# Kernel optimization log

Measured on AMD Instinct MI355X. Metric: run time of the kernel, lower is better.

The kernel has to match this reference:

```python
import jax, jax.numpy as jnp
import numpy as np

N_NODES = 100000
N_EDGES = 1600000
N_GRAPHS = 1024
IN_CH = 64
HID = 32
H4, H2 = HID * 4, HID * 2


def _glorot(key, shape):
    fan_in, fan_out = shape[0], shape[1]
    lim = (6.0 / (fan_in + fan_out)) ** 0.5
    return jax.random.uniform(key, shape, jnp.float32, -lim, lim)


def setup_inputs() -> dict:
    key = jax.random.key(0)
    ks = jax.random.split(key, 32)
    inp = {
        "x": jax.random.normal(ks[0], (N_NODES, IN_CH), jnp.float32),
        "edge_index": jax.random.randint(ks[1], (2, N_EDGES), 0, N_NODES, jnp.int64),
        "batch": jnp.sort(jax.random.randint(ks[2], (N_NODES,), 0, N_GRAPHS, jnp.int64)),
    }
    dims = [(IN_CH, H4), (H4, H2), (H2, H2), (H2, H2)]
    for i, (di, do) in enumerate(dims, 1):
        inp[f"c{i}_wl"] = _glorot(ks[3 * i], (di, do))
        inp[f"c{i}_bl"] = jnp.zeros((do,), jnp.float32)
        inp[f"c{i}_wr"] = _glorot(ks[3 * i + 1], (di, do))
    lin_dims = [(H2, H2), (H2, HID), (HID, HID), (HID, 1)]
    for i, (di, do) in enumerate(lin_dims, 1):
        inp[f"lin{i}_w"] = _glorot(ks[15 + 2 * i], (di, do))
        inp[f"lin{i}_b"] = jnp.zeros((do,), jnp.float32)
    return inp


def _sage(x, src, dst, wl, bl, wr):
    # mean-aggregate neighbor (source) features at target nodes
    agg = jax.ops.segment_sum(x[src], dst, num_segments=N_NODES)
    deg = jax.ops.segment_sum(jnp.ones((src.shape[0],), x.dtype), dst, num_segments=N_NODES)
    agg = agg / jnp.maximum(deg, 1.0)[:, None]
    return agg @ wl + bl + x @ wr


def reference(x, edge_index, batch,
              c1_wl, c1_bl, c1_wr, c2_wl, c2_bl, c2_wr,
              c3_wl, c3_bl, c3_wr, c4_wl, c4_bl, c4_wr,
              lin1_w, lin1_b, lin2_w, lin2_b, lin3_w, lin3_b, lin4_w, lin4_b):
    src, dst = edge_index[0], edge_index[1]
    h = jax.nn.relu(_sage(x, src, dst, c1_wl, c1_bl, c1_wr))
    h = jax.nn.relu(_sage(h, src, dst, c2_wl, c2_bl, c2_wr))
    h = jax.nn.relu(_sage(h, src, dst, c3_wl, c3_bl, c3_wr))
    h = jax.nn.relu(_sage(h, src, dst, c4_wl, c4_bl, c4_wr))
    # global mean pool over graphs
    gsum = jax.ops.segment_sum(h, batch, num_segments=N_GRAPHS)
    gcnt = jax.ops.segment_sum(jnp.ones((h.shape[0],), h.dtype), batch, num_segments=N_GRAPHS)
    g = gsum / jnp.maximum(gcnt, 1.0)[:, None]
    g = jax.nn.relu(g @ lin1_w + lin1_b)
    g = jax.nn.relu(g @ lin2_w + lin2_b)
    g = jax.nn.relu(g @ lin3_w + lin3_b)
    out = (g @ lin4_w + lin4_b).squeeze(1)  # [N_GRAPHS]
    return out
```

## Files before the change

### kernel.cpp

```cpp
#include <hip/hip_runtime.h>

#define NN 100000
#define NE 1600000
#define NG 1024
#define CPAD 4
#define MAXDEG 64

#define GB_COUNT 6250
#define GB_Z     1563
#define GB_CVT   3125
#define GB_BND   5
#define GB_PREP  320
#define GB_SETUP (2 * GB_COUNT)

typedef __attribute__((ext_vector_type(8))) short bf16x8;
typedef __attribute__((ext_vector_type(4))) float f32x4;

__device__ __forceinline__ unsigned f2bf1(float f) {
  union { float f; unsigned u; } v; v.f = f;
  return (v.u + 0x7fffu + ((v.u >> 16) & 1u)) >> 16;
}
__device__ __forceinline__ unsigned packbf2(float a, float b) {
  return f2bf1(a) | (f2bf1(b) << 16);
}
__device__ __forceinline__ float bflo(unsigned u) {
  union { unsigned u; float f; } v; v.u = u << 16; return v.f;
}
__device__ __forceinline__ float bfhi(unsigned u) {
  union { unsigned u; float f; } v; v.u = u & 0xffff0000u; return v.f;
}
__device__ __forceinline__ float bfs(unsigned short s) {
  union { unsigned u; float f; } v; v.u = ((unsigned)s) << 16; return v.f;
}

#define ACC16(A, P0, P1)                                              \
  A[0] += bflo(P0.x); A[1] += bfhi(P0.x);                             \
  A[2] += bflo(P0.y); A[3] += bfhi(P0.y);                             \
  A[4] += bflo(P0.z); A[5] += bfhi(P0.z);                             \
  A[6] += bflo(P0.w); A[7] += bfhi(P0.w);                             \
  A[8] += bflo(P1.x); A[9] += bfhi(P1.x);                             \
  A[10] += bflo(P1.y); A[11] += bfhi(P1.y);                           \
  A[12] += bflo(P1.z); A[13] += bfhi(P1.z);                           \
  A[14] += bflo(P1.w); A[15] += bfhi(P1.w);

#define ACC8(A, V)                                                    \
  A[0] += bflo(V.x); A[1] += bfhi(V.x);                               \
  A[2] += bflo(V.y); A[3] += bfhi(V.y);                               \
  A[4] += bflo(V.z); A[5] += bfhi(V.z);                               \
  A[6] += bflo(V.w); A[7] += bfhi(V.w);

__global__ __launch_bounds__(256) void k_prepz(const float* __restrict__ c1wr,
                                               unsigned short* __restrict__ pLZ) {
  int e = blockIdx.x * 256 + threadIdx.x;
  if (e >= 64 * 128) return;
  int k = e >> 7, n = e & 127;
  int t = k >> 5, kq = (k >> 3) & 3, j = k & 7;
  int n0 = n >> 4, nl = n & 15;
  pLZ[((((n0 * 2 + t) * 64) + (kq * 16 + nl)) << 3) + j] =
      (unsigned short)f2bf1(c1wr[k * 128 + n]);
}

__global__ __launch_bounds__(256) void k_setup(
    const int* __restrict__ src, const int* __restrict__ dst,
    int* __restrict__ cnt, int* __restrict__ csr,
    const float* __restrict__ X, unsigned short* __restrict__ Xb,
    const int* __restrict__ batch, int* __restrict__ gstart,
    const unsigned short* __restrict__ pLZ, const float* __restrict__ c1bl,
    unsigned short* __restrict__ ZZ,
    const float* __restrict__ c1wl, const float* __restrict__ c1wr,
    const float* __restrict__ c2wl, const float* __restrict__ c2wr,
    const float* __restrict__ c3wl, const float* __restrict__ c3wr,
    const float* __restrict__ c4wl, const float* __restrict__ c4wr,
    unsigned short* __restrict__ pL1, unsigned short* __restrict__ pL2a,
    unsigned short* __restrict__ pL2b, unsigned short* __restrict__ pL3,
    unsigned short* __restrict__ pL4) {
  __shared__ __align__(16) char smem[64 * 66 * 4];
  int b = blockIdx.x, tid = threadIdx.x;

  if ((b & 1) == 0) {
    int e = (b >> 1) * 256 + tid;
    int d = dst[e];
    int s = src[e];
    int r = atomicAdd(&cnt[(size_t)d * CPAD], 1);
    if (r < MAXDEG) csr[d * MAXDEG + r] = s;
    return;
  }
  int ob = b >> 1;

  if (ob < GB_Z) {
    unsigned short* sA = (unsigned short*)smem;
    float* sC = (float*)smem;
    const int m0 = ob * 64;
#pragma unroll
    for (int l = 0; l < 2; ++l) {
      int c = tid + l * 256;
      int m = c >> 3, k8 = c & 7;
      int row = m0 + m;
      uint4 o = make_uint4(0, 0, 0, 0);
      if (row < NN) {
        const float4* xp = (const float4*)(X + (size_t)row * 64 + k8 * 8);
        float4 p0 = xp[0], p1 = xp[1];
        o.x = packbf2(p0.x, p0.y); o.y = packbf2(p0.z, p0.w);
        o.z = packbf2(p1.x, p1.y); o.w = packbf2(p1.z, p1.w);
      }
      int wv = m >> 4, mr = m & 15, t = k8 >> 2, kq = k8 & 3;
      ((uint4*)sA)[(wv * 2 + t) * 64 + kq * 16 + mr] = o;
    }
    __syncthreads();
    const int w = tid >> 6, L = tid & 63;
    const bf16x8* Af = (const bf16x8*)sA;
    const bf16x8* Bf = (const bf16x8*)pLZ;
    f32x4 acc[8];
#pragma unroll
    for (int i = 0; i < 8; ++i)
#pragma unroll
      for (int j = 0; j < 4; ++j) acc[i][j] = 0.f;
#pragma unroll
    for (int t = 0; t < 2; ++t) {
      bf16x8 afr = Af[(w * 2 + t) * 64 + L];
#pragma unroll
      for (int n0 = 0; n0 < 8; ++n0) {
        bf16x8 bfr = Bf[(n0 * 2 + t) * 64 + L];
        acc[n0] = __builtin_amdgcn_mfma_f32_16x16x32_bf16(afr, bfr, acc[n0], 0, 0, 0);
      }
    }
    int rg = L >> 4, cl = L & 15;
#pragma unroll
    for (int half = 0; half < 2; ++half) {
      __syncthreads();
#pragma unroll
      for (int n0 = 0; n0 < 4; ++n0)
#pragma unroll
        for (int r = 0; r < 4; ++r)
          sC[(w * 16 + rg * 4 + r) * 66 + n0 * 16 + cl] = acc[half * 4 + n0][r];
      __syncthreads();
#pragma unroll
      for (int it = 0; it < 2; ++it) {
        int c = tid + it * 256;
        int m = c >> 3, c8 = c & 7;
        int row = m0 + m;
        if (row < NN) {
          float v[8];
#pragma unroll
          for (int j = 0; j < 8; ++j)
            v[j] = sC[m * 66 + c8 * 8 + j] + c1bl[half * 64 + c8 * 8 + j];
          uint4 o;
          o.x = packbf2(v[0], v[1]); o.y = packbf2(v[2], v[3]);
          o.z = packbf2(v[4], v[5]); o.w = packbf2(v[6], v[7]);
          ((uint4*)(ZZ + (size_t)row * 128 + half * 64))[c8] = o;
        }
      }
    }
    return;
  }
  ob -= GB_Z;
  if (ob < GB_CVT) {
    int i = ob * 256 + tid;
    const float4* p = (const float4*)X + (size_t)i * 2;
    float4 a = p[0], c = p[1];
    uint4 o;
    o.x = packbf2(a.x, a.y); o.y = packbf2(a.z, a.w);
    o.z = packbf2(c.x, c.y); o.w = packbf2(c.z, c.w);
    ((uint4*)Xb)[i] = o;
    return;
  }
  ob -= GB_CVT;
  if (ob < GB_BND) {
    int g = ob * 256 + tid;
    if (g > NG) return;
    int lo = 0, hi = NN;
    while (lo < hi) {
      int mid = (lo + hi) >> 1;
      if (batch[mid] < g) lo = mid + 1; else hi = mid;
    }
    gstart[g] = lo;
    return;
  }
  ob -= GB_BND;
  if (ob < GB_PREP) {
    int yb = ob >> 6, xb = ob & 63;
    const float *WL, *WR; unsigned short* dstp; int N;
    if (yb == 0)      { WL = c1wl; WR = c1wr;           dstp = pL1;  N = 128; }
    else if (yb == 1) { WL = c2wl; WR = c2wl + 64 * 64; dstp = pL2a; N = 64; }
    else if (yb == 2) { WL = c2wr; WR = c2wr + 64 * 64; dstp = pL2b; N = 64; }
    else if (yb == 3) { WL = c3wl; WR = c3wr;           dstp = pL3;  N = 64; }
    else              { WL = c4wl; WR = c4wr;           dstp = pL4;  N = 64; }
    int e = xb * 256 + tid;
    if (e >= 128 * N) return;
    int k = e / N, n = e - k * N;
    float w = (k < 64) ? WL[k * N + n] : WR[(k - 64) * N + n];
    int t = k >> 5, kq = (k >> 3) & 3, j = k & 7;
    int n0 = n >> 4, nl = n & 15;
    dstp[((((n0 * 4 + t) * 64) + (kq * 16 + nl)) << 3) + j] =
        (unsigned short)f2bf1(w);
  }
}

__global__ __launch_bounds__(256) void k_gather(
    const unsigned short* __restrict__ F, const int* __restrict__ csr,
    const int* __restrict__ cnt, const float* __restrict__ bias,
    const unsigned short* __restrict__ Z, unsigned short* __restrict__ out) {
  int idx = blockIdx.x * 256 + threadIdx.x;
  int n = idx >> 3, q = idx & 7;
  int deg = cnt[(size_t)n * CPAD];
  int degc = min(deg, MAXDEG);
  int beg = n * MAXDEG, end = beg + degc;
  float aA[8], aB[8];
#pragma unroll
  for (int c = 0; c < 8; ++c) { aA[c] = 0.f; aB[c] = 0.f; }
  int e = beg;
  for (; e + 8 <= end; e += 8) {
    int4 s0 = *(const int4*)(csr + e);
    int4 s1 = *(const int4*)(csr + e + 4);
    uint4 v0 = ((const uint4*)(F + (size_t)s0.x * 64))[q];
    uint4 v1 = ((const uint4*)(F + (size_t)s0.y * 64))[q];
    uint4 v2 = ((const uint4*)(F + (size_t)s0.z * 64))[q];
    uint4 v3 = ((const uint4*)(F + (size_t)s0.w * 64))[q];
    uint4 v4 = ((const uint4*)(F + (size_t)s1.x * 64))[q];
    uint4 v5 = ((const uint4*)(F + (size_t)s1.y * 64))[q];
    uint4 v6 = ((const uint4*)(F + (size_t)s1.z * 64))[q];
    uint4 v7 = ((const uint4*)(F + (size_t)s1.w * 64))[q];
    ACC8(aA, v0) ACC8(aB, v1) ACC8(aA, v2) ACC8(aB, v3)
    ACC8(aA, v4) ACC8(aB, v5) ACC8(aA, v6) ACC8(aB, v7)
  }
  if (e + 4 <= end) {
    int4 s0 = *(const int4*)(csr + e);
    uint4 v0 = ((const uint4*)(F + (size_t)s0.x * 64))[q];
    uint4 v1 = ((const uint4*)(F + (size_t)s0.y * 64))[q];
    uint4 v2 = ((const uint4*)(F + (size_t)s0.z * 64))[q];
    uint4 v3 = ((const uint4*)(F + (size_t)s0.w * 64))[q];
    ACC8(aA, v0) ACC8(aB, v1) ACC8(aA, v2) ACC8(aB, v3)
    e += 4;
  }
  for (; e < end; ++e) {
    uint4 v0 = ((const uint4*)(F + (size_t)csr[e] * 64))[q];
    ACC8(aA, v0)
  }
  float a[8];
  float iv = 1.0f / fmaxf((float)deg, 1.0f);
#pragma unroll
  for (int c = 0; c < 8; ++c) a[c] = (aA[c] + aB[c]) * iv;
  {
    uint4 z = ((const uint4*)(Z + (size_t)n * 64))[q];
    const float4* bp = (const float4*)(bias + q * 8);
    float4 b0 = bp[0], b1 = bp[1];
    a[0] = fmaxf(a[0] + b0.x + bflo(z.x), 0.f);
    a[1] = fmaxf(a[1] + b0.y + bfhi(z.x), 0.f);
    a[2] = fmaxf(a[2] + b0.z + bflo(z.y), 0.f);
    a[3] = fmaxf(a[3] + b0.w + bfhi(z.y), 0.f);
    a[4] = fmaxf(a[4] + b1.x + bflo(z.z), 0.f);
    a[5] = fmaxf(a[5] + b1.y + bfhi(z.z), 0.f);
    a[6] = fmaxf(a[6] + b1.z + bflo(z.w), 0.f);
    a[7] = fmaxf(a[7] + b1.w + bfhi(z.w), 0.f);
  }
  uint4 o;
  o.x = packbf2(a[0], a[1]); o.y = packbf2(a[2], a[3]);
  o.z = packbf2(a[4], a[5]); o.w = packbf2(a[6], a[7]);
  ((uint4*)(out + (size_t)n * 64))[q] = o;
}

__device__ __forceinline__ void gather_row(
    const unsigned short* __restrict__ F, const int* __restrict__ csr,
    const int* __restrict__ cnt, int row, int qr, float* a0) {
  float a1[16];
#pragma unroll
  for (int c = 0; c < 16; ++c) { a0[c] = 0.f; a1[c] = 0.f; }
  int deg = cnt[(size_t)row * CPAD];
  int degc = min(deg, MAXDEG);
  int beg = row * MAXDEG, end = beg + degc;
  int e = beg;
  for (; e + 4 <= end; e += 4) {
    int4 ss = *(const int4*)(csr + e);
    const uint4* r0 = (const uint4*)(F + (size_t)ss.x * 64) + qr * 2;
    const uint4* r1 = (const uint4*)(F + (size_t)ss.y * 64) + qr * 2;
    const uint4* r2 = (const uint4*)(F + (size_t)ss.z * 64) + qr * 2;
    const uint4* r3 = (const uint4*)(F + (size_t)ss.w * 64) + qr * 2;
    uint4 p0 = r0[0], p1 = r0[1], q0 = r1[0], q1 = r1[1];
    uint4 p2 = r2[0], p3 = r2[1], q2 = r3[0], q3 = r3[1];
    ACC16(a0, p0, p1) ACC16(a1, q0, q1)
    ACC16(a0, p2, p3) ACC16(a1, q2, q3)
  }
  if (e + 2 <= end) {
    int s0 = csr[e], s1 = csr[e + 1];
    const uint4* r0 = (const uint4*)(F + (size_t)s0 * 64) + qr * 2;
    const uint4* r1 = (const uint4*)(F + (size_t)s1 * 64) + qr * 2;
    uint4 p0 = r0[0], p1 = r0[1], q0 = r1[0], q1 = r1[1];
    ACC16(a0, p0, p1) ACC16(a1, q0, q1)
    e += 2;
  }
  if (e < end) {
    const uint4* r0 = (const uint4*)(F + (size_t)csr[e] * 64) + qr * 2;
    uint4 p0 = r0[0], p1 = r0[1];
    ACC16(a0, p0, p1)
  }
  float iv = 1.0f / fmaxf((float)deg, 1.0f);
#pragma unroll
  for (int c = 0; c < 16; ++c) a0[c] = (a0[c] + a1[c]) * iv;
}

__global__ __launch_bounds__(256, 4) void k_fgemm1(
    const unsigned short* __restrict__ F, const int* __restrict__ csr,
    const int* __restrict__ cnt,
    const unsigned short* __restrict__ Wp,
    const unsigned short* __restrict__ ZZ,
    const unsigned short* __restrict__ Wa,
    const unsigned short* __restrict__ Wb,
    unsigned short* __restrict__ OUTa,
    unsigned short* __restrict__ OUTb) {
  __shared__ __align__(16) char smem[64 * 66 * 4 + 64 * 128 * 2];
  unsigned short* sA = (unsigned short*)smem;
  float* sC = (float*)smem;
  unsigned short* sA2 = (unsigned short*)(smem + 64 * 66 * 4);
  const int tid = threadIdx.x;
  const int m0 = blockIdx.x * 64;

  {
    int m = tid >> 2, qr = tid & 3;
    int row = m0 + m;
    float a0[16];
    if (row < NN) {
      gather_row(F, csr, cnt, row, qr, a0);
    } else {
#pragma unroll
      for (int c = 0; c < 16; ++c) a0[c] = 0.f;
    }
    int wv = m >> 4, mr = m & 15;
#pragma unroll
    for (int h = 0; h < 2; ++h) {
      int k8 = qr * 2 + h;
      int t = k8 >> 2, kq = k8 & 3;
      uint4 o;
      o.x = packbf2(a0[h * 8 + 0], a0[h * 8 + 1]);
      o.y = packbf2(a0[h * 8 + 2], a0[h * 8 + 3]);
      o.z = packbf2(a0[h * 8 + 4], a0[h * 8 + 5]);
      o.w = packbf2(a0[h * 8 + 6], a0[h * 8 + 7]);
      ((uint4*)sA)[(wv * 2 + t) * 64 + kq * 16 + mr] = o;
    }
  }
  __syncthreads();

  const int w = tid >> 6, L = tid & 63;
  const bf16x8* Af = (const bf16x8*)sA;
  const bf16x8* Bf = (const bf16x8*)Wp;
  f32x4 acc[8];
#pragma unroll
  for (int i = 0; i < 8; ++i)
#pragma unroll
    for (int j = 0; j < 4; ++j) acc[i][j] = 0.f;
#pragma unroll
  for (int t = 0; t < 2; ++t) {
    bf16x8 afr = Af[(w * 2 + t) * 64 + L];
#pragma unroll
    for (int n0 = 0; n0 < 8; ++n0) {
      bf16x8 bfr = Bf[(n0 * 4 + t) * 64 + L];
      acc[n0] = __builtin_amdgcn_mfma_f32_16x16x32_bf16(afr, bfr, acc[n0], 0, 0, 0);
    }
  }

  int rg = L >> 4, cl = L & 15;
#pragma unroll
  for (int half = 0; half < 2; ++half) {
    __syncthreads();
#pragma unroll
    for (int n0 = 0; n0 < 4; ++n0)
#pragma unroll
      for (int r = 0; r < 4; ++r)
        sC[(w * 16 + rg * 4 + r) * 66 + n0 * 16 + cl] = acc[half * 4 + n0][r];
    __syncthreads();
#pragma unroll
    for (int it = 0; it < 2; ++it) {
      int c = tid + it * 256;
      int m = c >> 3, c8 = c & 7;
      int row = m0 + m;
      uint4 o = make_uint4(0, 0, 0, 0);
      if (row < NN) {
        uint4 z = ((const uint4*)(ZZ + (size_t)row * 128 + half * 64))[c8];
        float zb[8] = {bflo(z.x), bfhi(z.x), bflo(z.y), bfhi(z.y),
                       bflo(z.z), bfhi(z.z), bflo(z.w), bfhi(z.w)};
        float v[8];
#pragma unroll
        for (int j = 0; j < 8; ++j)
          v[j] = fmaxf(sC[m * 66 + c8 * 8 + j] + zb[j], 0.f);
        o.x = packbf2(v[0], v[1]); o.y = packbf2(v[2], v[3]);
        o.z = packbf2(v[4], v[5]); o.w = packbf2(v[6], v[7]);
      }
      int k8 = half * 8 + c8, t = k8 >> 2, kq = k8 & 3;
      int wv = m >> 4, mr = m & 15;
      ((uint4*)sA2)[(wv * 4 + t) * 64 + kq * 16 + mr] = o;
    }
  }
  __syncthreads();

  const bf16x8* A2 = (const bf16x8*)sA2;
  const bf16x8* Ba = (const bf16x8*)Wa;
  const bf16x8* Bb = (const bf16x8*)Wb;
  f32x4 ca[4], cb[4];
#pragma unroll
  for (int i = 0; i < 4; ++i)
#pragma unroll
    for (int j = 0; j < 4; ++j) { ca[i][j] = 0.f; cb[i][j] = 0.f; }
#pragma unroll
  for (int t = 0; t < 4; ++t) {
    bf16x8 afr = A2[(w * 4 + t) * 64 + L];
#pragma unroll
    for (int n0 = 0; n0 < 4; ++n0) {
      ca[n0] = __builtin_amdgcn_mfma_f32_16x16x32_bf16(afr, Ba[(n0 * 4 + t) * 64 + L], ca[n0], 0, 0, 0);
      cb[n0] = __builtin_amdgcn_mfma_f32_16x16x32_bf16(afr, Bb[(n0 * 4 + t) * 64 + L], cb[n0], 0, 0, 0);
    }
  }
#pragma unroll
  for (int s = 0; s < 2; ++s) {
    unsigned short* OUT = s ? OUTb : OUTa;
    __syncthreads();
#pragma unroll
    for (int n0 = 0; n0 < 4; ++n0)
#pragma unroll
      for (int r = 0; r < 4; ++r)
        sC[(w * 16 + rg * 4 + r) * 66 + n0 * 16 + cl] =
            s ? cb[n0][r] : ca[n0][r];
    __syncthreads();
#pragma unroll
    for (int it = 0; it < 2; ++it) {
      int c = tid + it * 256;
      int m = c >> 3, c8 = c & 7;
      int row = m0 + m;
      if (row < NN) {
        float v[8];
#pragma unroll
        for (int j = 0; j < 8; ++j) v[j] = sC[m * 66 + c8 * 8 + j];
        uint4 o;
        o.x = packbf2(v[0], v[1]); o.y = packbf2(v[2], v[3]);
        o.z = packbf2(v[4], v[5]); o.w = packbf2(v[6], v[7]);
        ((uint4*)(OUT + (size_t)row * 64))[c8] = o;
      }
    }
  }
}

template <int NF>
__global__ __launch_bounds__(256, 4) void k_fgemm(
    const unsigned short* __restrict__ F, const int* __restrict__ csr,
    const int* __restrict__ cnt,
    const unsigned short* __restrict__ Wp, const float* __restrict__ bias,
    unsigned short* __restrict__ OUT, int outStride) {
  __shared__ __align__(16) char smem[64 * 66 * 4];
  unsigned short* sA = (unsigned short*)smem;
  float* sC = (float*)smem;
  const int tid = threadIdx.x;
  const int m0 = blockIdx.x * 64;

  {
    int m = tid >> 2, qr = tid & 3;
    int row = m0 + m;
    float a0[16];
    if (row < NN) {
      gather_row(F, csr, cnt, row, qr, a0);
    } else {
#pragma unroll
      for (int c = 0; c < 16; ++c) a0[c] = 0.f;
    }
    int wv = m >> 4, mr = m & 15;
#pragma unroll
    for (int h = 0; h < 2; ++h) {
      int k8 = qr * 2 + h;
      int t = k8 >> 2, kq = k8 & 3;
      uint4 o;
      o.x = packbf2(a0[h * 8 + 0], a0[h * 8 + 1]);
      o.y = packbf2(a0[h * 8 + 2], a0[h * 8 + 3]);
      o.z = packbf2(a0[h * 8 + 4], a0[h * 8 + 5]);
      o.w = packbf2(a0[h * 8 + 6], a0[h * 8 + 7]);
      ((uint4*)sA)[(wv * 4 + t) * 64 + kq * 16 + mr] = o;
    }
  }
#pragma unroll
  for (int l = 0; l < 2; ++l) {
    int c = tid + l * 256;
    int m = c >> 3, j = c & 7;
    int row = m0 + m;
    uint4 v = make_uint4(0, 0, 0, 0);
    if (row < NN) v = ((const uint4*)(F + (size_t)row * 64))[j];
    int k8 = 8 + j, t = k8 >> 2, kq = k8 & 3;
    int wv = m >> 4, mr = m & 15;
    ((uint4*)sA)[(wv * 4 + t) * 64 + kq * 16 + mr] = v;
  }
  __syncthreads();

  const int w = tid >> 6, L = tid & 63;
  const bf16x8* Af = (const bf16x8*)sA;
  const bf16x8* Bf = (const bf16x8*)Wp;
  f32x4 acc[NF];
#pragma unroll
  for (int i = 0; i < NF; ++i)
#pragma unroll
    for (int j = 0; j < 4; ++j) acc[i][j] = 0.f;
#pragma unroll
  for (int t = 0; t < 4; ++t) {
    bf16x8 afr = Af[(w * 4 + t) * 64 + L];
#pragma unroll
    for (int n0 = 0; n0 < NF; ++n0) {
      bf16x8 bfr = Bf[(n0 * 4 + t) * 64 + L];
      acc[n0] = __builtin_amdgcn_mfma_f32_16x16x32_bf16(afr, bfr, acc[n0], 0, 0, 0);
    }
  }

  int rg = L >> 4, cl = L & 15;
#pragma unroll
  for (int half = 0; half < NF / 4; ++half) {
    __syncthreads();
#pragma unroll
    for (int n0 = 0; n0 < 4; ++n0)
#pragma unroll
      for (int r = 0; r < 4; ++r)
        sC[(w * 16 + rg * 4 + r) * 66 + n0 * 16 + cl] = acc[half * 4 + n0][r];
    __syncthreads();
#pragma unroll
    for (int it = 0; it < 2; ++it) {
      int c = tid + it * 256;
      int m = c >> 3, c8 = c & 7;
      int row = m0 + m;
      if (row < NN) {
        float v[8];
#pragma unroll
        for (int j = 0; j < 8; ++j)
          v[j] = fmaxf(sC[m * 66 + c8 * 8 + j] + bias[half * 64 + c8 * 8 + j], 0.f);
        uint4 o;
        o.x = packbf2(v[0], v[1]); o.y = packbf2(v[2], v[3]);
        o.z = packbf2(v[4], v[5]); o.w = packbf2(v[6], v[7]);
        ((uint4*)(OUT + (size_t)row * outStride + half * 64))[c8] = o;
      }
    }
  }
}

__global__ __launch_bounds__(64) void k_poolmlp(
    const unsigned short* __restrict__ H, const int* __restrict__ gstart,
    const float* __restrict__ w1, const float* __restrict__ b1,
    const float* __restrict__ w2, const float* __restrict__ b2,
    const float* __restrict__ w3, const float* __restrict__ b3,
    const float* __restrict__ w4, const float* __restrict__ b4,
    float* __restrict__ out) {
  __shared__ float sg[64], s1[64], s2[32], s3[32];
  int g = blockIdx.x, t = threadIdx.x;
  int beg = gstart[g], end = gstart[g + 1];
  float acc = 0.0f;
#pragma unroll 4
  for (int n = beg; n < end; ++n) acc += bfs(H[(size_t)n * 64 + t]);
  float cnt = fmaxf((float)(end - beg), 1.0f);
  sg[t] = acc / cnt;
  __syncthreads();
  acc = b1[t];
  for (int k = 0; k < 64; ++k) acc += sg[k] * w1[k * 64 + t];
  s1[t] = fmaxf(acc, 0.0f);
  __syncthreads();
  if (t < 32) {
    acc = b2[t];
    for (int k = 0; k < 64; ++k) acc += s1[k] * w2[k * 32 + t];
    s2[t] = fmaxf(acc, 0.0f);
  }
  __syncthreads();
  if (t < 32) {
    acc = b3[t];
    for (int k = 0; k < 32; ++k) acc += s2[k] * w3[k * 32 + t];
    s3[t] = fmaxf(acc, 0.0f);
  }
  __syncthreads();
  if (t == 0) {
    acc = b4[0];
    for (int k = 0; k < 32; ++k) acc += s3[k] * w4[k];
    out[g] = acc;
  }
}

extern "C" void kernel_launch(void* const* d_in, const int* in_sizes, int n_in,
                              void* d_out, int out_size, void* d_ws,
                              size_t ws_size, hipStream_t stream) {
  const float* x     = (const float*)d_in[0];
  const int*   ei    = (const int*)d_in[1];
  const int*   batch = (const int*)d_in[2];
  const int* src = ei;
  const int* dst = ei + NE;

  const float* c1_wl = (const float*)d_in[3];
  const float* c1_bl = (const float*)d_in[4];
  const float* c1_wr = (const float*)d_in[5];
  const float* c2_wl = (const float*)d_in[6];
  const float* c2_bl = (const float*)d_in[7];
  const float* c2_wr = (const float*)d_in[8];
  const float* c3_wl = (const float*)d_in[9];
  const float* c3_bl = (const float*)d_in[10];
  const float* c3_wr = (const float*)d_in[11];
  const float* c4_wl = (const float*)d_in[12];
  const float* c4_bl = (const float*)d_in[13];
  const float* c4_wr = (const float*)d_in[14];
  const float* l1w = (const float*)d_in[15];
  const float* l1b = (const float*)d_in[16];
  const float* l2w = (const float*)d_in[17];
  const float* l2b = (const float*)d_in[18];
  const float* l3w = (const float*)d_in[19];
  const float* l3b = (const float*)d_in[20];
  const float* l4w = (const float*)d_in[21];
  const float* l4b = (const float*)d_in[22];

  char* wsb = (char*)d_ws;
  unsigned short* xb  = (unsigned short*)wsb;
  unsigned short* B1  = xb + (size_t)NN * 64;
  unsigned short* B3  = B1 + (size_t)NN * 64;
  unsigned short* B4  = B3 + (size_t)NN * 64;
  unsigned short* ZZ  = B4 + (size_t)NN * 64;
  unsigned short* pL1  = ZZ + (size_t)NN * 128;
  unsigned short* pL2a = pL1 + 128 * 128;
  unsigned short* pL2b = pL2a + 128 * 64;
  unsigned short* pL3  = pL2b + 128 * 64;
  unsigned short* pL4  = pL3 + 128 * 64;
  unsigned short* pLZ  = pL4 + 128 * 64;
  int* cnt    = (int*)(pLZ + 64 * 128);
  int* gstart = cnt + (size_t)NN * CPAD;
  int* csr    = gstart + NG + 1 + 2;

  const int gN8 = NN * 8 / 256;
  const int gM  = (NN + 63) / 64;

  hipMemsetAsync(cnt, 0, (size_t)NN * CPAD * 4, stream);

  k_prepz<<<32, 256, 0, stream>>>(c1_wr, pLZ);

  k_setup<<<GB_SETUP, 256, 0, stream>>>(src, dst, cnt, csr, x, xb, batch,
                                        gstart, pLZ, c1_bl, ZZ,
                                        c1_wl, c1_wr, c2_wl, c2_wr,
                                        c3_wl, c3_wr, c4_wl, c4_wr,
                                        pL1, pL2a, pL2b, pL3, pL4);

  k_fgemm1<<<gM, 256, 0, stream>>>(xb, csr, cnt, pL1, ZZ, pL2a, pL2b, B3, B4);

  k_gather<<<gN8, 256, 0, stream>>>(B3, csr, cnt, c2_bl, B4, B1);

  k_fgemm<4><<<gM, 256, 0, stream>>>(B1, csr, cnt, pL3, c3_bl, B3, 64);

  k_fgemm<4><<<gM, 256, 0, stream>>>(B3, csr, cnt, pL4, c4_bl, B1, 64);

  k_poolmlp<<<NG, 64, 0, stream>>>(B1, gstart, l1w, l1b, l2w, l2b,
                                   l3w, l3b, l4w, l4b, (float*)d_out);
}
```

Measured before the change: 352.2 us.

## Batch edge CSR build per block, widen gather unroll, split pool accumulators

After: 375.1 us. 1.07x slower.

```diff
diff --git a/kernel.cpp b/kernel.cpp
--- a/kernel.cpp
+++ b/kernel.cpp
@@ -6,12 +6,13 @@
 #define CPAD 4
 #define MAXDEG 64
 
-#define GB_COUNT 6250
+#define GB_COUNT 1563
 #define GB_Z     1563
 #define GB_CVT   3125
 #define GB_BND   5
 #define GB_PREP  320
-#define GB_SETUP (2 * GB_COUNT)
+#define GB_ODD   (GB_Z + GB_CVT + GB_BND + GB_PREP)
+#define GB_SETUP 6684
 
 typedef __attribute__((ext_vector_type(8))) short bf16x8;
 typedef __attribute__((ext_vector_type(4))) float f32x4;
@@ -77,15 +78,26 @@
   __shared__ __align__(16) char smem[64 * 66 * 4];
   int b = blockIdx.x, tid = threadIdx.x;
 
-  if ((b & 1) == 0) {
-    int e = (b >> 1) * 256 + tid;
-    int d = dst[e];
-    int s = src[e];
-    int r = atomicAdd(&cnt[(size_t)d * CPAD], 1);
-    if (r < MAXDEG) csr[d * MAXDEG + r] = s;
+  if ((b & 3) == 0) {
+    int cb = b >> 2;
+    if (cb >= GB_COUNT) return;
+    int base = cb * 1024 + tid;
+    int dd[4], ss[4];
+#pragma unroll
+    for (int k = 0; k < 4; ++k) {
+      int e = base + k * 256;
+      if (e < NE) { dd[k] = dst[e]; ss[k] = src[e]; } else dd[k] = -1;
+    }
+#pragma unroll
+    for (int k = 0; k < 4; ++k) {
+      if (dd[k] >= 0) {
+        int r = atomicAdd(&cnt[(size_t)dd[k] * CPAD], 1);
+        if (r < MAXDEG) csr[dd[k] * MAXDEG + r] = ss[k];
+      }
+    }
     return;
   }
-  int ob = b >> 1;
+  int ob = (b >> 2) * 3 + (b & 3) - 1;
 
   if (ob < GB_Z) {
     unsigned short* sA = (unsigned short*)smem;
@@ -262,30 +274,50 @@
 __device__ __forceinline__ void gather_row(
     const unsigned short* __restrict__ F, const int* __restrict__ csr,
     const int* __restrict__ cnt, int row, int qr, float* a0) {
-  float a1[16];
-#pragma unroll
-  for (int c = 0; c < 16; ++c) { a0[c] = 0.f; a1[c] = 0.f; }
+#pragma unroll
+  for (int c = 0; c < 16; ++c) a0[c] = 0.f;
   int deg = cnt[(size_t)row * CPAD];
   int degc = min(deg, MAXDEG);
   int beg = row * MAXDEG, end = beg + degc;
   int e = beg;
-  for (; e + 4 <= end; e += 4) {
-    int4 ss = *(const int4*)(csr + e);
-    const uint4* r0 = (const uint4*)(F + (size_t)ss.x * 64) + qr * 2;
-    const uint4* r1 = (const uint4*)(F + (size_t)ss.y * 64) + qr * 2;
-    const uint4* r2 = (const uint4*)(F + (size_t)ss.z * 64) + qr * 2;
-    const uint4* r3 = (const uint4*)(F + (size_t)ss.w * 64) + qr * 2;
-    uint4 p0 = r0[0], p1 = r0[1], q0 = r1[0], q1 = r1[1];
-    uint4 p2 = r2[0], p3 = r2[1], q2 = r3[0], q3 = r3[1];
-    ACC16(a0, p0, p1) ACC16(a1, q0, q1)
-    ACC16(a0, p2, p3) ACC16(a1, q2, q3)
+  for (; e + 8 <= end; e += 8) {
+    int4 sa = *(const int4*)(csr + e);
+    int4 sb = *(const int4*)(csr + e + 4);
+    const uint4* r0 = (const uint4*)(F + (size_t)sa.x * 64) + qr * 2;
+    const uint4* r1 = (const uint4*)(F + (size_t)sa.y * 64) + qr * 2;
+    const uint4* r2 = (const uint4*)(F + (size_t)sa.z * 64) + qr * 2;
+    const uint4* r3 = (const uint4*)(F + (size_t)sa.w * 64) + qr * 2;
+    const uint4* r4 = (const uint4*)(F + (size_t)sb.x * 64) + qr * 2;
+    const uint4* r5 = (const uint4*)(F + (size_t)sb.y * 64) + qr * 2;
+    const uint4* r6 = (const uint4*)(F + (size_t)sb.z * 64) + qr * 2;
+    const uint4* r7 = (const uint4*)(F + (size_t)sb.w * 64) + qr * 2;
+    uint4 p0 = r0[0], p1 = r0[1], p2 = r1[0], p3 = r1[1];
+    uint4 p4 = r2[0], p5 = r2[1], p6 = r3[0], p7 = r3[1];
+    uint4 q0 = r4[0], q1 = r4[1], q2 = r5[0], q3 = r5[1];
+    uint4 q4 = r6[0], q5 = r6[1], q6 = r7[0], q7 = r7[1];
+    ACC16(a0, p0, p1) ACC16(a0, p2, p3)
+    ACC16(a0, p4, p5) ACC16(a0, p6, p7)
+    ACC16(a0, q0, q1) ACC16(a0, q2, q3)
+    ACC16(a0, q4, q5) ACC16(a0, q6, q7)
+  }
+  if (e + 4 <= end) {
+    int4 sa = *(const int4*)(csr + e);
+    const uint4* r0 = (const uint4*)(F + (size_t)sa.x * 64) + qr * 2;
+    const uint4* r1 = (const uint4*)(F + (size_t)sa.y * 64) + qr * 2;
+    const uint4* r2 = (const uint4*)(F + (size_t)sa.z * 64) + qr * 2;
+    const uint4* r3 = (const uint4*)(F + (size_t)sa.w * 64) + qr * 2;
+    uint4 p0 = r0[0], p1 = r0[1], p2 = r1[0], p3 = r1[1];
+    uint4 p4 = r2[0], p5 = r2[1], p6 = r3[0], p7 = r3[1];
+    ACC16(a0, p0, p1) ACC16(a0, p2, p3)
+    ACC16(a0, p4, p5) ACC16(a0, p6, p7)
+    e += 4;
   }
   if (e + 2 <= end) {
     int s0 = csr[e], s1 = csr[e + 1];
     const uint4* r0 = (const uint4*)(F + (size_t)s0 * 64) + qr * 2;
     const uint4* r1 = (const uint4*)(F + (size_t)s1 * 64) + qr * 2;
     uint4 p0 = r0[0], p1 = r0[1], q0 = r1[0], q1 = r1[1];
-    ACC16(a0, p0, p1) ACC16(a1, q0, q1)
+    ACC16(a0, p0, p1) ACC16(a0, q0, q1)
     e += 2;
   }
   if (e < end) {
@@ -295,7 +327,7 @@
   }
   float iv = 1.0f / fmaxf((float)deg, 1.0f);
 #pragma unroll
-  for (int c = 0; c < 16; ++c) a0[c] = (a0[c] + a1[c]) * iv;
+  for (int c = 0; c < 16; ++c) a0[c] *= iv;
 }
 
 __global__ __launch_bounds__(256, 4) void k_fgemm1(
@@ -542,13 +574,19 @@
   __shared__ float sg[64], s1[64], s2[32], s3[32];
   int g = blockIdx.x, t = threadIdx.x;
   int beg = gstart[g], end = gstart[g + 1];
-  float acc = 0.0f;
-#pragma unroll 4
-  for (int n = beg; n < end; ++n) acc += bfs(H[(size_t)n * 64 + t]);
+  float a0 = 0.f, a1 = 0.f, a2 = 0.f, a3 = 0.f;
+  int n = beg;
+  for (; n + 4 <= end; n += 4) {
+    a0 += bfs(H[(size_t)n * 64 + t]);
+    a1 += bfs(H[(size_t)(n + 1) * 64 + t]);
+    a2 += bfs(H[(size_t)(n + 2) * 64 + t]);
+    a3 += bfs(H[(size_t)(n + 3) * 64 + t]);
+  }
+  for (; n < end; ++n) a0 += bfs(H[(size_t)n * 64 + t]);
   float cnt = fmaxf((float)(end - beg), 1.0f);
-  sg[t] = acc / cnt;
+  sg[t] = ((a0 + a1) + (a2 + a3)) / cnt;
   __syncthreads();
-  acc = b1[t];
+  float acc = b1[t];
   for (int k = 0; k < 64; ++k) acc += sg[k] * w1[k * 64 + t];
   s1[t] = fmaxf(acc, 0.0f);
   __syncthreads();
```
